# Kernel optimization log

Measured on AMD Instinct MI355X. Metric: run time of the kernel, lower is better.

The kernel has to match this reference:

```python
import jax, jax.numpy as jnp
import numpy as np

N_NODES = 50000
N_EDGES = 1_600_000


def gcn_conv(x, W, b, src, dst, ew, n_nodes):
    """PyG GCNConv: out = D^{-1/2}(A+I)D^{-1/2} (x W) + b, deg from edge_weight,
    self-loop weight = 1. Self-loop term handled analytically (norm = dinv[i]^2)."""
    xW = x @ W                                            # [N, F_out]
    deg = jax.ops.segment_sum(ew, dst, num_segments=n_nodes) + 1.0  # +1 self-loop
    dinv = jnp.where(deg > 0, jax.lax.rsqrt(deg), 0.0)    # [N]
    norm = dinv[src] * ew * dinv[dst]                     # [E]
    agg = jax.ops.segment_sum(norm[:, None] * xW[src], dst, num_segments=n_nodes)
    return agg + (dinv * dinv)[:, None] * xW + b


def setup_inputs() -> dict:
    key = jax.random.key(0)
    ks = jax.random.split(key, 9)
    s = lambda fi, fo: 1.0 / np.sqrt(fi)
    return {
        "x": jax.random.normal(ks[0], (N_NODES, 128), dtype=jnp.float32),
        "edge_index": jax.random.randint(ks[1], (2, N_EDGES), 0, N_NODES, dtype=jnp.int64)
        if jax.config.jax_enable_x64 else jax.random.randint(ks[1], (2, N_EDGES), 0, N_NODES, dtype=jnp.int32),
        "edge_weight": jax.random.uniform(ks[2], (N_EDGES,), dtype=jnp.float32),
        "W1": jax.random.normal(ks[3], (128, 64), dtype=jnp.float32) * s(128, 64),
        "b1": jnp.zeros((64,), dtype=jnp.float32),
        "W2": jax.random.normal(ks[4], (64, 64), dtype=jnp.float32) * s(64, 64),
        "b2": jnp.zeros((64,), dtype=jnp.float32),
        "W3": jax.random.normal(ks[5], (64, 40), dtype=jnp.float32) * s(64, 40),
        "b3": jnp.zeros((40,), dtype=jnp.float32),
    }


def reference(x, edge_index, edge_weight, W1, b1, W2, b2, W3, b3):
    src, dst = edge_index[0], edge_index[1]
    n = x.shape[0]
    h = jax.nn.relu(gcn_conv(x, W1, b1, src, dst, edge_weight, n))
    h = jax.nn.relu(gcn_conv(h, W2, b2, src, dst, edge_weight, n))
    return gcn_conv(h, W3, b3, src, dst, edge_weight, n)
```

## Files before the change

### kernel.cpp

```cpp
#include <hip/hip_runtime.h>


#define TILE 4096
#define BCAP_MAX 9216

static __device__ __forceinline__ float4 f4zero() { return make_float4(0.f, 0.f, 0.f, 0.f); }

static __device__ __forceinline__ unsigned short f2bf_rne(float x) {
    unsigned u = __float_as_uint(x);
    u += 0x7FFFu + ((u >> 16) & 1u);
    return (unsigned short)(u >> 16);
}
static __device__ __forceinline__ float bflo(unsigned u) { return __uint_as_float(u << 16); }
static __device__ __forceinline__ float bfhi(unsigned u) { return __uint_as_float(u & 0xffff0000u); }

__global__ __launch_bounds__(1024) void bin_count_kernel(
        const int* __restrict__ dst, int* __restrict__ cnt, int E, int ntiles) {
    __shared__ int h[256];
    const int tid = threadIdx.x;
    const int t = blockIdx.x;
    if (tid < 256) h[tid] = 0;
    __syncthreads();
    const int e0 = t * TILE;
    #pragma unroll
    for (int j = 0; j < 4; ++j) {
        int e = e0 + j * 1024 + tid;
        if (e < E) atomicAdd(&h[dst[e] >> 8], 1);
    }
    __syncthreads();
    if (tid < 256) cnt[tid * ntiles + t] = h[tid];
}

__global__ __launch_bounds__(512) void bin_scan_kernel(
        int* __restrict__ cnt, int* __restrict__ bintotal, int ntiles) {
    __shared__ int buf[512];
    const int b = blockIdx.x;
    const int tid = threadIdx.x;
    int v = (tid < ntiles) ? cnt[b * ntiles + tid] : 0;
    buf[tid] = v;
    __syncthreads();
    for (int off = 1; off < 512; off <<= 1) {
        int x = buf[tid];
        int a = (tid >= off) ? buf[tid - off] : 0;
        __syncthreads();
        buf[tid] = x + a;
        __syncthreads();
    }
    if (tid < ntiles) cnt[b * ntiles + tid] = buf[tid] - v;
    if (tid == 0) bintotal[b] = buf[511];
}

__global__ __launch_bounds__(1024) void bin_scatter_kernel(
        const int* __restrict__ src, const int* __restrict__ dst,
        const float* __restrict__ ew, const int* __restrict__ cntbase,
        int2* __restrict__ binned, int E, int bcap, int ntiles) {
    __shared__ int cnt[256];
    __shared__ int scan[256];
    __shared__ int gbase[256];
    __shared__ int2 sorted[TILE];
    __shared__ unsigned char binof[TILE];
    const int tid = threadIdx.x;
    const int t = blockIdx.x;
    const int e0 = t * TILE;

    if (tid < 256) cnt[tid] = 0;
    __syncthreads();

    int mypk[4]; float myew[4]; int mybin[4]; int myrank[4]; bool myok[4];
    #pragma unroll
    for (int j = 0; j < 4; ++j) {
        int e = e0 + j * 1024 + tid;
        myok[j] = (e < E);
        if (myok[j]) {
            int d = dst[e];
            int s = src[e];
            myew[j]   = ew[e];
            mybin[j]  = d >> 8;
            mypk[j]   = (s << 8) | (d & 255);
            myrank[j] = atomicAdd(&cnt[mybin[j]], 1);
        }
    }
    __syncthreads();
    if (tid < 256) scan[tid] = cnt[tid];
    __syncthreads();
    for (int off = 1; off < 256; off <<= 1) {
        int v = 0;
        if (tid < 256) { v = scan[tid]; if (tid >= off) v += scan[tid - off]; }
        __syncthreads();
        if (tid < 256) scan[tid] = v;
        __syncthreads();
    }
    if (tid < 256) gbase[tid] = cntbase[tid * ntiles + t];
    __syncthreads();
    #pragma unroll
    for (int j = 0; j < 4; ++j) {
        if (myok[j]) {
            int b = mybin[j];
            int slot = (scan[b] - cnt[b]) + myrank[j];
            sorted[slot] = make_int2(mypk[j], __float_as_int(myew[j]));
            binof[slot]  = (unsigned char)b;
        }
    }
    __syncthreads();
    const int total = scan[255];
    for (int i = tid; i < total; i += 1024) {
        int b = binof[i];
        int pos = gbase[b] + (i - (scan[b] - cnt[b]));
        if (pos < bcap)
            binned[(size_t)b * bcap + pos] = sorted[i];
    }
}

__global__ __launch_bounds__(1024) void bin_group_kernel(
        int2* __restrict__ binned, const int* __restrict__ bintotal,
        int* __restrict__ row_start, int* __restrict__ row_cnt,
        float* __restrict__ dinv, int N, int bcap) {
    __shared__ int   cntl[256];
    __shared__ float degl[256];
    __shared__ int   scan[256];
    __shared__ int   run[256];
    __shared__ int2  sorted[BCAP_MAX];
    const int b = blockIdx.x;
    const int tid = threadIdx.x;
    int n = bintotal[b];
    if (n > bcap) n = bcap;
    if (tid < 256) { cntl[tid] = 0; degl[tid] = 0.f; }
    __syncthreads();

    int2* seg = binned + (size_t)b * bcap;
    for (int i = tid; i < n; i += 1024) {
        int2 v = seg[i];
        int dl = v.x & 255;
        atomicAdd(&cntl[dl], 1);
        atomicAdd(&degl[dl], __int_as_float(v.y));
    }
    __syncthreads();
    if (tid < 256) scan[tid] = cntl[tid];
    __syncthreads();
    for (int off = 1; off < 256; off <<= 1) {
        int v = 0;
        if (tid < 256) { v = scan[tid]; if (tid >= off) v += scan[tid - off]; }
        __syncthreads();
        if (tid < 256) scan[tid] = v;
        __syncthreads();
    }
    if (tid < 256) {
        int ex = scan[tid] - cntl[tid];
        int d = (b << 8) + tid;
        if (d < N) {
            row_start[d] = b * bcap + ex;
            row_cnt[d]   = cntl[tid];
            dinv[d]      = rsqrtf(degl[tid] + 1.0f);
        }
        run[tid] = ex;
    }
    __syncthreads();
    for (int i = tid; i < n; i += 1024) {
        int2 v = seg[i];
        int dl = v.x & 255;
        int r = atomicAdd(&run[dl], 1);
        sorted[r] = make_int2((v.x >> 8) << 7, v.y);
    }
    __syncthreads();
    for (int i = tid; i < n; i += 1024)
        seg[i] = sorted[i];
}

template <int K, int M>
__global__ __launch_bounds__(256) void gemm_kernel(const float* __restrict__ X,
        const float* __restrict__ W, const float* __restrict__ dinv,
        unsigned short* __restrict__ Y, int N) {
    constexpr int KP = K + 4;
    __shared__ float xs[64 * KP];
    __shared__ float ws[K * M];
    const int tid = threadIdx.x;
    const int row0 = blockIdx.x * 64;

    for (int i = tid * 4; i < K * M; i += 1024)
        *(float4*)&ws[i] = *(const float4*)&W[i];

    const int nrows = min(64, N - row0);
    for (int i = tid * 4; i < 64 * K; i += 1024) {
        int r = i / K, k = i % K;
        float4 v = f4zero();
        if (r < nrows) v = *(const float4*)&X[(size_t)(row0 + r) * K + k];
        *(float4*)&xs[r * KP + k] = v;
    }
    __syncthreads();

    const int ct = tid & 15, rt = tid >> 4;
    const int c = ct * 4;
    const bool cok = (c < M);
    float acc[4][4] = {};
    for (int k = 0; k < K; ++k) {
        float a0 = xs[(rt +  0) * KP + k];
        float a1 = xs[(rt + 16) * KP + k];
        float a2 = xs[(rt + 32) * KP + k];
        float a3 = xs[(rt + 48) * KP + k];
        float4 bv = cok ? *(const float4*)&ws[k * M + c] : f4zero();
        acc[0][0] += a0 * bv.x; acc[0][1] += a0 * bv.y; acc[0][2] += a0 * bv.z; acc[0][3] += a0 * bv.w;
        acc[1][0] += a1 * bv.x; acc[1][1] += a1 * bv.y; acc[1][2] += a1 * bv.z; acc[1][3] += a1 * bv.w;
        acc[2][0] += a2 * bv.x; acc[2][1] += a2 * bv.y; acc[2][2] += a2 * bv.z; acc[2][3] += a2 * bv.w;
        acc[3][0] += a3 * bv.x; acc[3][1] += a3 * bv.y; acc[3][2] += a3 * bv.z; acc[3][3] += a3 * bv.w;
    }
    if (cok) {
        #pragma unroll
        for (int i = 0; i < 4; ++i) {
            int r = row0 + rt + 16 * i;
            if (r < N) {
                float dd = dinv[r];
                ushort4 o;
                o.x = f2bf_rne(acc[i][0] * dd); o.y = f2bf_rne(acc[i][1] * dd);
                o.z = f2bf_rne(acc[i][2] * dd); o.w = f2bf_rne(acc[i][3] * dd);
                *(ushort4*)&Y[(size_t)r * 64 + c] = o;
            }
        }
    }
}

template <int FOUT, bool RELU>
__global__ __launch_bounds__(256) void agg_kernel(
        const unsigned short* __restrict__ xw,
        const int2* __restrict__ csr, const int* __restrict__ row_start,
        const int* __restrict__ row_cnt, const float* __restrict__ dinv,
        const float* __restrict__ bias, float* __restrict__ out, int N) {
    int wid = (int)((blockIdx.x * blockDim.x + threadIdx.x) >> 6);
    int lane = threadIdx.x & 63;
    if (wid >= N) return;

    const int2* row = csr + row_start[wid];
    const int   cnt = row_cnt[wid];
    const char* xwb = (const char*)xw;

    const int g = lane >> 3;
    const unsigned li16 = (unsigned)(lane & 7) * 16u;
    const int g4 = g << 2;

    float acc[8] = {0.f, 0.f, 0.f, 0.f, 0.f, 0.f, 0.f, 0.f};

    int2 edA = make_int2(0, 0);
    if (lane < cnt) edA = row[lane];

    for (int base = 0; base < cnt; base += 64) {
        const int m = min(cnt - base, 64);
        int2 edN = make_int2(0, 0);
        const int nb = base + 64;
        if (nb < cnt) {
            if (lane < cnt - nb) edN = row[nb + lane];
        }
        int bidx = g4;
        #pragma unroll 2
        for (int t = 0; t * 8 < m; ++t, bidx += 32) {
            unsigned off = (unsigned)__builtin_amdgcn_ds_bpermute(bidx, edA.x);
            unsigned wu  = (unsigned)__builtin_amdgcn_ds_bpermute(bidx, edA.y);
            const bool valid = (t * 8 + g) < m;
            off = valid ? off : 0u;
            float wf = valid ? __uint_as_float(wu) : 0.f;
            uint4 rv = *(const uint4*)(xwb + (size_t)(off + li16));
            acc[0] = fmaf(wf, bflo(rv.x), acc[0]);
            acc[1] = fmaf(wf, bfhi(rv.x), acc[1]);
            acc[2] = fmaf(wf, bflo(rv.y), acc[2]);
            acc[3] = fmaf(wf, bfhi(rv.y), acc[3]);
            acc[4] = fmaf(wf, bflo(rv.z), acc[4]);
            acc[5] = fmaf(wf, bfhi(rv.z), acc[5]);
            acc[6] = fmaf(wf, bflo(rv.w), acc[6]);
            acc[7] = fmaf(wf, bfhi(rv.w), acc[7]);
        }
        edA = edN;
    }

    #pragma unroll
    for (int o = 8; o <= 32; o <<= 1) {
        #pragma unroll
        for (int t = 0; t < 8; ++t)
            acc[t] += __shfl_xor(acc[t], o);
    }

    if (lane < FOUT / 8) {
        const int f0 = lane * 8;
        uint4 sr = *(const uint4*)(xwb + ((unsigned)wid * 128u + li16));
        float dd = dinv[wid];
        float4 bv0 = *(const float4*)&bias[f0];
        float4 bv1 = *(const float4*)&bias[f0 + 4];
        float r0 = dd * (acc[0] + bflo(sr.x)) + bv0.x;
        float r1 = dd * (acc[1] + bfhi(sr.x)) + bv0.y;
        float r2 = dd * (acc[2] + bflo(sr.y)) + bv0.z;
        float r3 = dd * (acc[3] + bfhi(sr.y)) + bv0.w;
        float r4 = dd * (acc[4] + bflo(sr.z)) + bv1.x;
        float r5 = dd * (acc[5] + bfhi(sr.z)) + bv1.y;
        float r6 = dd * (acc[6] + bflo(sr.w)) + bv1.z;
        float r7 = dd * (acc[7] + bfhi(sr.w)) + bv1.w;
        if (RELU) {
            r0 = fmaxf(r0, 0.f); r1 = fmaxf(r1, 0.f); r2 = fmaxf(r2, 0.f); r3 = fmaxf(r3, 0.f);
            r4 = fmaxf(r4, 0.f); r5 = fmaxf(r5, 0.f); r6 = fmaxf(r6, 0.f); r7 = fmaxf(r7, 0.f);
        }
        *(float4*)&out[(size_t)wid * FOUT + f0]     = make_float4(r0, r1, r2, r3);
        *(float4*)&out[(size_t)wid * FOUT + f0 + 4] = make_float4(r4, r5, r6, r7);
    }
}

static inline size_t ws_align(size_t x) { return (x + 255) & ~(size_t)255; }

extern "C" void kernel_launch(void* const* d_in, const int* in_sizes, int n_in,
                              void* d_out, int out_size, void* d_ws, size_t ws_size,
                              hipStream_t stream) {
    const float* x  = (const float*)d_in[0];
    const int*   ei = (const int*)d_in[1];
    const float* ew = (const float*)d_in[2];
    const float* W1 = (const float*)d_in[3];
    const float* b1 = (const float*)d_in[4];
    const float* W2 = (const float*)d_in[5];
    const float* b2 = (const float*)d_in[6];
    const float* W3 = (const float*)d_in[7];
    const float* b3 = (const float*)d_in[8];
    float* out = (float*)d_out;

    const int N = in_sizes[0] / 128;
    const int E = in_sizes[1] / 2;
    const int* src = ei;
    const int* dst = ei + E;
    const int nbins = (N + 255) >> 8;
    const int ntiles = (E + TILE - 1) / TILE;

    char* p = (char*)d_ws;
    size_t off = 0;
    auto alloc = [&](size_t bytes) -> char* {
        char* q = p + off;
        off = ws_align(off + bytes);
        return q;
    };
    int*   row_start = (int*)  alloc((size_t)N * 4);
    int*   row_cnt   = (int*)  alloc((size_t)N * 4);
    float* dinv      = (float*)alloc((size_t)N * 4);
    int*   cntbase   = (int*)  alloc((size_t)256 * ntiles * 4);
    int*   bintotal  = (int*)  alloc((size_t)256 * 4);
    unsigned short* xwbuf = (unsigned short*)alloc((size_t)N * 64 * 2);
    float* hbuf      = (float*)alloc((size_t)N * 64 * 4);
    size_t remain = (ws_size > off + 512) ? (ws_size - off - 512) : 0;
    int bcap = (int)(remain / ((size_t)nbins * 8));
    if (bcap > BCAP_MAX) bcap = BCAP_MAX;
    int2* binned = (int2*)alloc((size_t)nbins * (size_t)bcap * 8);

    const int gb = (N + 63) / 64;
    const int ab = (N + 3) / 4;

    bin_count_kernel<<<ntiles, 1024, 0, stream>>>(dst, cntbase, E, ntiles);
    bin_scan_kernel<<<256, 512, 0, stream>>>(cntbase, bintotal, ntiles);
    bin_scatter_kernel<<<ntiles, 1024, 0, stream>>>(src, dst, ew, cntbase, binned, E, bcap, ntiles);
    bin_group_kernel<<<nbins, 1024, 0, stream>>>(binned, bintotal, row_start, row_cnt, dinv, N, bcap);

    gemm_kernel<128, 64><<<gb, 256, 0, stream>>>(x, W1, dinv, xwbuf, N);
    agg_kernel<64, true ><<<ab, 256, 0, stream>>>(xwbuf, binned, row_start, row_cnt, dinv, b1, hbuf, N);
    gemm_kernel<64, 64><<<gb, 256, 0, stream>>>(hbuf, W2, dinv, xwbuf, N);
    agg_kernel<64, true ><<<ab, 256, 0, stream>>>(xwbuf, binned, row_start, row_cnt, dinv, b2, hbuf, N);
    gemm_kernel<64, 40><<<gb, 256, 0, stream>>>(hbuf, W3, dinv, xwbuf, N);
    agg_kernel<40, false><<<ab, 256, 0, stream>>>(xwbuf, binned, row_start, row_cnt, dinv, b3, out, N);
}
```

Measured before the change: 269.3 us.

## Replace two-level bin sort with global-atomic CSR build

Replaces the tiled two-level binning (shared-memory histograms, per-bin scan, local scatter and regroup) with a direct CSR construction: global atomic count and degree per node, a single-block exclusive scan, and an atomic-slot scatter. The goal is fewer kernels, fewer passes over the edge list and no capacity-limited bins. In exchange it relies on heavy global atomics to random addresses, a serial one-block scan over all nodes, and edge order within each row that varies from run to run, so float summation order is not deterministic.

```diff
diff --git a/kernel.cpp b/kernel.cpp
--- a/kernel.cpp
+++ b/kernel.cpp
@@ -1,8 +1,5 @@
 #include <hip/hip_runtime.h>
 
-
-#define TILE 4096
-#define BCAP_MAX 9216
 
 static __device__ __forceinline__ float4 f4zero() { return make_float4(0.f, 0.f, 0.f, 0.f); }
 
@@ -14,156 +11,67 @@
 static __device__ __forceinline__ float bflo(unsigned u) { return __uint_as_float(u << 16); }
 static __device__ __forceinline__ float bfhi(unsigned u) { return __uint_as_float(u & 0xffff0000u); }
 
-__global__ __launch_bounds__(1024) void bin_count_kernel(
-        const int* __restrict__ dst, int* __restrict__ cnt, int E, int ntiles) {
-    __shared__ int h[256];
+__global__ __launch_bounds__(1024) void zero_kernel(int* __restrict__ cnt,
+        float* __restrict__ deg, int N) {
+    int i = blockIdx.x * 1024 + threadIdx.x;
+    if (i < N) { cnt[i] = 0; deg[i] = 0.f; }
+}
+
+__global__ __launch_bounds__(1024) void count_kernel(
+        const int* __restrict__ dst, const float* __restrict__ ew,
+        int* __restrict__ cnt, float* __restrict__ deg, int E) {
+    int stride = gridDim.x * 1024;
+    for (int e = blockIdx.x * 1024 + threadIdx.x; e < E; e += stride) {
+        int d = dst[e];
+        atomicAdd(&cnt[d], 1);
+        atomicAdd(&deg[d], ew[e]);
+    }
+}
+
+__global__ __launch_bounds__(1024) void scan_kernel(
+        const int* __restrict__ cnt, const float* __restrict__ deg,
+        int* __restrict__ row_start, int* __restrict__ run,
+        float* __restrict__ dinv, int N) {
+    __shared__ int buf[1024];
     const int tid = threadIdx.x;
-    const int t = blockIdx.x;
-    if (tid < 256) h[tid] = 0;
+    const int P = (N + 1023) >> 10;
+    int s = 0;
+    for (int i = 0; i < P; ++i) {
+        int idx = i * 1024 + tid;
+        if (idx < N) s += cnt[idx];
+    }
+    buf[tid] = s;
     __syncthreads();
-    const int e0 = t * TILE;
-    #pragma unroll
-    for (int j = 0; j < 4; ++j) {
-        int e = e0 + j * 1024 + tid;
-        if (e < E) atomicAdd(&h[dst[e] >> 8], 1);
-    }
-    __syncthreads();
-    if (tid < 256) cnt[tid * ntiles + t] = h[tid];
-}
-
-__global__ __launch_bounds__(512) void bin_scan_kernel(
-        int* __restrict__ cnt, int* __restrict__ bintotal, int ntiles) {
-    __shared__ int buf[512];
-    const int b = blockIdx.x;
-    const int tid = threadIdx.x;
-    int v = (tid < ntiles) ? cnt[b * ntiles + tid] : 0;
-    buf[tid] = v;
-    __syncthreads();
-    for (int off = 1; off < 512; off <<= 1) {
+    for (int off = 1; off < 1024; off <<= 1) {
         int x = buf[tid];
         int a = (tid >= off) ? buf[tid - off] : 0;
         __syncthreads();
         buf[tid] = x + a;
         __syncthreads();
     }
-    if (tid < ntiles) cnt[b * ntiles + tid] = buf[tid] - v;
-    if (tid == 0) bintotal[b] = buf[511];
-}
-
-__global__ __launch_bounds__(1024) void bin_scatter_kernel(
+    int r = buf[tid] - s;
+    for (int i = 0; i < P; ++i) {
+        int idx = i * 1024 + tid;
+        if (idx < N) {
+            int c = cnt[idx];
+            row_start[idx] = r;
+            run[idx]       = r;
+            dinv[idx]      = rsqrtf(deg[idx] + 1.0f);
+            r += c;
+        }
+    }
+}
+
+__global__ __launch_bounds__(1024) void scatter_kernel(
         const int* __restrict__ src, const int* __restrict__ dst,
-        const float* __restrict__ ew, const int* __restrict__ cntbase,
-        int2* __restrict__ binned, int E, int bcap, int ntiles) {
-    __shared__ int cnt[256];
-    __shared__ int scan[256];
-    __shared__ int gbase[256];
-    __shared__ int2 sorted[TILE];
-    __shared__ unsigned char binof[TILE];
-    const int tid = threadIdx.x;
-    const int t = blockIdx.x;
-    const int e0 = t * TILE;
-
-    if (tid < 256) cnt[tid] = 0;
-    __syncthreads();
-
-    int mypk[4]; float myew[4]; int mybin[4]; int myrank[4]; bool myok[4];
-    #pragma unroll
-    for (int j = 0; j < 4; ++j) {
-        int e = e0 + j * 1024 + tid;
-        myok[j] = (e < E);
-        if (myok[j]) {
-            int d = dst[e];
-            int s = src[e];
-            myew[j]   = ew[e];
-            mybin[j]  = d >> 8;
-            mypk[j]   = (s << 8) | (d & 255);
-            myrank[j] = atomicAdd(&cnt[mybin[j]], 1);
-        }
-    }
-    __syncthreads();
-    if (tid < 256) scan[tid] = cnt[tid];
-    __syncthreads();
-    for (int off = 1; off < 256; off <<= 1) {
-        int v = 0;
-        if (tid < 256) { v = scan[tid]; if (tid >= off) v += scan[tid - off]; }
-        __syncthreads();
-        if (tid < 256) scan[tid] = v;
-        __syncthreads();
-    }
-    if (tid < 256) gbase[tid] = cntbase[tid * ntiles + t];
-    __syncthreads();
-    #pragma unroll
-    for (int j = 0; j < 4; ++j) {
-        if (myok[j]) {
-            int b = mybin[j];
-            int slot = (scan[b] - cnt[b]) + myrank[j];
-            sorted[slot] = make_int2(mypk[j], __float_as_int(myew[j]));
-            binof[slot]  = (unsigned char)b;
-        }
-    }
-    __syncthreads();
-    const int total = scan[255];
-    for (int i = tid; i < total; i += 1024) {
-        int b = binof[i];
-        int pos = gbase[b] + (i - (scan[b] - cnt[b]));
-        if (pos < bcap)
-            binned[(size_t)b * bcap + pos] = sorted[i];
-    }
-}
-
-__global__ __launch_bounds__(1024) void bin_group_kernel(
-        int2* __restrict__ binned, const int* __restrict__ bintotal,
-        int* __restrict__ row_start, int* __restrict__ row_cnt,
-        float* __restrict__ dinv, int N, int bcap) {
-    __shared__ int   cntl[256];
-    __shared__ float degl[256];
-    __shared__ int   scan[256];
-    __shared__ int   run[256];
-    __shared__ int2  sorted[BCAP_MAX];
-    const int b = blockIdx.x;
-    const int tid = threadIdx.x;
-    int n = bintotal[b];
-    if (n > bcap) n = bcap;
-    if (tid < 256) { cntl[tid] = 0; degl[tid] = 0.f; }
-    __syncthreads();
-
-    int2* seg = binned + (size_t)b * bcap;
-    for (int i = tid; i < n; i += 1024) {
-        int2 v = seg[i];
-        int dl = v.x & 255;
-        atomicAdd(&cntl[dl], 1);
-        atomicAdd(&degl[dl], __int_as_float(v.y));
-    }
-    __syncthreads();
-    if (tid < 256) scan[tid] = cntl[tid];
-    __syncthreads();
-    for (int off = 1; off < 256; off <<= 1) {
-        int v = 0;
-        if (tid < 256) { v = scan[tid]; if (tid >= off) v += scan[tid - off]; }
-        __syncthreads();
-        if (tid < 256) scan[tid] = v;
-        __syncthreads();
-    }
-    if (tid < 256) {
-        int ex = scan[tid] - cntl[tid];
-        int d = (b << 8) + tid;
-        if (d < N) {
-            row_start[d] = b * bcap + ex;
-            row_cnt[d]   = cntl[tid];
-            dinv[d]      = rsqrtf(degl[tid] + 1.0f);
-        }
-        run[tid] = ex;
-    }
-    __syncthreads();
-    for (int i = tid; i < n; i += 1024) {
-        int2 v = seg[i];
-        int dl = v.x & 255;
-        int r = atomicAdd(&run[dl], 1);
-        sorted[r] = make_int2((v.x >> 8) << 7, v.y);
-    }
-    __syncthreads();
-    for (int i = tid; i < n; i += 1024)
-        seg[i] = sorted[i];
+        const float* __restrict__ ew, int* __restrict__ run,
+        int2* __restrict__ binned, int E) {
+    int stride = gridDim.x * 1024;
+    for (int e = blockIdx.x * 1024 + threadIdx.x; e < E; e += stride) {
+        int d = dst[e];
+        int pos = atomicAdd(&run[d], 1);
+        binned[pos] = make_int2(src[e] << 7, __float_as_int(ew[e]));
+    }
 }
 
 template <int K, int M>
@@ -319,8 +227,6 @@
     const int E = in_sizes[1] / 2;
     const int* src = ei;
     const int* dst = ei + E;
-    const int nbins = (N + 255) >> 8;
-    const int ntiles = (E + TILE - 1) / TILE;
 
     char* p = (char*)d_ws;
     size_t off = 0;
@@ -331,23 +237,22 @@
     };
     int*   row_start = (int*)  alloc((size_t)N * 4);
     int*   row_cnt   = (int*)  alloc((size_t)N * 4);
+    int*   run       = (int*)  alloc((size_t)N * 4);
+    float* deg       = (float*)alloc((size_t)N * 4);
     float* dinv      = (float*)alloc((size_t)N * 4);
-    int*   cntbase   = (int*)  alloc((size_t)256 * ntiles * 4);
-    int*   bintotal  = (int*)  alloc((size_t)256 * 4);
     unsigned short* xwbuf = (unsigned short*)alloc((size_t)N * 64 * 2);
     float* hbuf      = (float*)alloc((size_t)N * 64 * 4);
-    size_t remain = (ws_size > off + 512) ? (ws_size - off - 512) : 0;
-    int bcap = (int)(remain / ((size_t)nbins * 8));
-    if (bcap > BCAP_MAX) bcap = BCAP_MAX;
-    int2* binned = (int2*)alloc((size_t)nbins * (size_t)bcap * 8);
-
+    int2*  binned    = (int2*) alloc((size_t)E * 8);
+
+    const int zb = (N + 1023) / 1024;
+    const int eb = 512;
     const int gb = (N + 63) / 64;
     const int ab = (N + 3) / 4;
 
-    bin_count_kernel<<<ntiles, 1024, 0, stream>>>(dst, cntbase, E, ntiles);
-    bin_scan_kernel<<<256, 512, 0, stream>>>(cntbase, bintotal, ntiles);
-    bin_scatter_kernel<<<ntiles, 1024, 0, stream>>>(src, dst, ew, cntbase, binned, E, bcap, ntiles);
-    bin_group_kernel<<<nbins, 1024, 0, stream>>>(binned, bintotal, row_start, row_cnt, dinv, N, bcap);
+    zero_kernel<<<zb, 1024, 0, stream>>>(row_cnt, deg, N);
+    count_kernel<<<eb, 1024, 0, stream>>>(dst, ew, row_cnt, deg, E);
+    scan_kernel<<<1, 1024, 0, stream>>>(row_cnt, deg, row_start, run, dinv, N);
+    scatter_kernel<<<eb, 1024, 0, stream>>>(src, dst, ew, run, binned, E);
 
     gemm_kernel<128, 64><<<gb, 256, 0, stream>>>(x, W1, dinv, xwbuf, N);
     agg_kernel<64, true ><<<ab, 256, 0, stream>>>(xwbuf, binned, row_start, row_cnt, dinv, b1, hbuf, N);
```

Result: slower. 533.5 us (+98.1%).

## Split bf16 XW into column planes and aggregate each plane in separate passes

Applied to the files above, without the earlier changes.

The GEMM output now goes into two column planes: the first 32 features, then the rest (32 or 8). Each layer's aggregation runs as two passes, one per plane, so each pass gathers a smaller working set (about 3.2 MB for 50k×32 bf16) that fits better in cache for the random neighbour gathers. Edge offsets are stored as row*64 and shifted per plane width. The cost is twice the CSR traversal and kernel launches per layer, and the 8-wide pass gives each lane less work.

```diff
diff --git a/kernel.cpp b/kernel.cpp
--- a/kernel.cpp
+++ b/kernel.cpp
@@ -159,7 +159,7 @@
         int2 v = seg[i];
         int dl = v.x & 255;
         int r = atomicAdd(&run[dl], 1);
-        sorted[r] = make_int2((v.x >> 8) << 7, v.y);
+        sorted[r] = make_int2((v.x >> 8) << 6, v.y);
     }
     __syncthreads();
     for (int i = tid; i < n; i += 1024)
@@ -171,6 +171,7 @@
         const float* __restrict__ W, const float* __restrict__ dinv,
         unsigned short* __restrict__ Y, int N) {
     constexpr int KP = K + 4;
+    constexpr int P1S = (M == 40) ? 8 : 32;
     __shared__ float xs[64 * KP];
     __shared__ float ws[K * M];
     const int tid = threadIdx.x;
@@ -212,29 +213,34 @@
                 ushort4 o;
                 o.x = f2bf_rne(acc[i][0] * dd); o.y = f2bf_rne(acc[i][1] * dd);
                 o.z = f2bf_rne(acc[i][2] * dd); o.w = f2bf_rne(acc[i][3] * dd);
-                *(ushort4*)&Y[(size_t)r * 64 + c] = o;
+                unsigned short* dp;
+                if (c < 32) dp = &Y[(size_t)r * 32 + c];
+                else        dp = &Y[(size_t)N * 32 + (size_t)r * P1S + (c - 32)];
+                *(ushort4*)dp = o;
             }
         }
     }
 }
 
-template <int FOUT, bool RELU>
-__global__ __launch_bounds__(256) void agg_kernel(
-        const unsigned short* __restrict__ xw,
+template <int FH, int FTOT, int COFF, bool RELU>
+__global__ __launch_bounds__(256) void agg_pass_kernel(
+        const unsigned short* __restrict__ plane,
         const int2* __restrict__ csr, const int* __restrict__ row_start,
         const int* __restrict__ row_cnt, const float* __restrict__ dinv,
         const float* __restrict__ bias, float* __restrict__ out, int N) {
+    constexpr int LPR = FH / 8;
+    constexpr int EPS = 64 / LPR;
+    constexpr int SH  = (FH == 32) ? 0 : 2;
     int wid = (int)((blockIdx.x * blockDim.x + threadIdx.x) >> 6);
     int lane = threadIdx.x & 63;
     if (wid >= N) return;
 
     const int2* row = csr + row_start[wid];
     const int   cnt = row_cnt[wid];
-    const char* xwb = (const char*)xw;
-
-    const int g = lane >> 3;
-    const unsigned li16 = (unsigned)(lane & 7) * 16u;
-    const int g4 = g << 2;
+    const char* xwb = (const char*)plane;
+
+    const int g = lane / LPR;
+    const unsigned li16 = (unsigned)(lane % LPR) * 16u;
 
     float acc[8] = {0.f, 0.f, 0.f, 0.f, 0.f, 0.f, 0.f, 0.f};
 
@@ -248,15 +254,22 @@
         if (nb < cnt) {
             if (lane < cnt - nb) edN = row[nb + lane];
         }
-        int bidx = g4;
-        #pragma unroll 2
-        for (int t = 0; t * 8 < m; ++t, bidx += 32) {
-            unsigned off = (unsigned)__builtin_amdgcn_ds_bpermute(bidx, edA.x);
-            unsigned wu  = (unsigned)__builtin_amdgcn_ds_bpermute(bidx, edA.y);
-            const bool valid = (t * 8 + g) < m;
+        #pragma unroll
+        for (int t = 0; t < 64 / EPS; ++t) {
+            if (t * EPS >= m) break;
+            unsigned off, wu;
+            if (EPS == 64) {
+                off = (unsigned)edA.x;
+                wu  = (unsigned)edA.y;
+            } else {
+                int bidx = (t * EPS + g) << 2;
+                off = (unsigned)__builtin_amdgcn_ds_bpermute(bidx, edA.x);
+                wu  = (unsigned)__builtin_amdgcn_ds_bpermute(bidx, edA.y);
+            }
+            const bool valid = (t * EPS + g) < m;
             off = valid ? off : 0u;
             float wf = valid ? __uint_as_float(wu) : 0.f;
-            uint4 rv = *(const uint4*)(xwb + (size_t)(off + li16));
+            uint4 rv = *(const uint4*)(xwb + (size_t)((off >> SH) + li16));
             acc[0] = fmaf(wf, bflo(rv.x), acc[0]);
             acc[1] = fmaf(wf, bfhi(rv.x), acc[1]);
             acc[2] = fmaf(wf, bflo(rv.y), acc[2]);
@@ -270,18 +283,18 @@
     }
 
     #pragma unroll
-    for (int o = 8; o <= 32; o <<= 1) {
+    for (int o = LPR; o <= 32; o <<= 1) {
         #pragma unroll
         for (int t = 0; t < 8; ++t)
             acc[t] += __shfl_xor(acc[t], o);
     }
 
-    if (lane < FOUT / 8) {
+    if (lane < LPR) {
         const int f0 = lane * 8;
-        uint4 sr = *(const uint4*)(xwb + ((unsigned)wid * 128u + li16));
+        uint4 sr = *(const uint4*)(xwb + (size_t)wid * (FH * 2) + (unsigned)lane * 16u);
         float dd = dinv[wid];
-        float4 bv0 = *(const float4*)&bias[f0];
-        float4 bv1 = *(const float4*)&bias[f0 + 4];
+        float4 bv0 = *(const float4*)&bias[COFF + f0];
+        float4 bv1 = *(const float4*)&bias[COFF + f0 + 4];
         float r0 = dd * (acc[0] + bflo(sr.x)) + bv0.x;
         float r1 = dd * (acc[1] + bfhi(sr.x)) + bv0.y;
         float r2 = dd * (acc[2] + bflo(sr.y)) + bv0.z;
@@ -294,8 +307,8 @@
             r0 = fmaxf(r0, 0.f); r1 = fmaxf(r1, 0.f); r2 = fmaxf(r2, 0.f); r3 = fmaxf(r3, 0.f);
             r4 = fmaxf(r4, 0.f); r5 = fmaxf(r5, 0.f); r6 = fmaxf(r6, 0.f); r7 = fmaxf(r7, 0.f);
         }
-        *(float4*)&out[(size_t)wid * FOUT + f0]     = make_float4(r0, r1, r2, r3);
-        *(float4*)&out[(size_t)wid * FOUT + f0 + 4] = make_float4(r4, r5, r6, r7);
+        *(float4*)&out[(size_t)wid * FTOT + COFF + f0]     = make_float4(r0, r1, r2, r3);
+        *(float4*)&out[(size_t)wid * FTOT + COFF + f0 + 4] = make_float4(r4, r5, r6, r7);
     }
 }
 
@@ -336,10 +349,12 @@
     int*   bintotal  = (int*)  alloc((size_t)256 * 4);
     unsigned short* xwbuf = (unsigned short*)alloc((size_t)N * 64 * 2);
     float* hbuf      = (float*)alloc((size_t)N * 64 * 4);
-    size_t remain = (ws_size > off + 512) ? (ws_size - off - 512) : 0;
+    size_t remain = (ws_size > off) ? (ws_size - off) : 0;
     int bcap = (int)(remain / ((size_t)nbins * 8));
     if (bcap > BCAP_MAX) bcap = BCAP_MAX;
     int2* binned = (int2*)alloc((size_t)nbins * (size_t)bcap * 8);
+
+    const unsigned short* plane1 = xwbuf + (size_t)N * 32;
 
     const int gb = (N + 63) / 64;
     const int ab = (N + 3) / 4;
@@ -350,9 +365,12 @@
     bin_group_kernel<<<nbins, 1024, 0, stream>>>(binned, bintotal, row_start, row_cnt, dinv, N, bcap);
 
     gemm_kernel<128, 64><<<gb, 256, 0, stream>>>(x, W1, dinv, xwbuf, N);
-    agg_kernel<64, true ><<<ab, 256, 0, stream>>>(xwbuf, binned, row_start, row_cnt, dinv, b1, hbuf, N);
+    agg_pass_kernel<32, 64,  0, true ><<<ab, 256, 0, stream>>>(xwbuf,  binned, row_start, row_cnt, dinv, b1, hbuf, N);
+    agg_pass_kernel<32, 64, 32, true ><<<ab, 256, 0, stream>>>(plane1, binned, row_start, row_cnt, dinv, b1, hbuf, N);
     gemm_kernel<64, 64><<<gb, 256, 0, stream>>>(hbuf, W2, dinv, xwbuf, N);
-    agg_kernel<64, true ><<<ab, 256, 0, stream>>>(xwbuf, binned, row_start, row_cnt, dinv, b2, hbuf, N);
+    agg_pass_kernel<32, 64,  0, true ><<<ab, 256, 0, stream>>>(xwbuf,  binned, row_start, row_cnt, dinv, b2, hbuf, N);
+    agg_pass_kernel<32, 64, 32, true ><<<ab, 256, 0, stream>>>(plane1, binned, row_start, row_cnt, dinv, b2, hbuf, N);
     gemm_kernel<64, 40><<<gb, 256, 0, stream>>>(hbuf, W3, dinv, xwbuf, N);
-    agg_kernel<40, false><<<ab, 256, 0, stream>>>(xwbuf, binned, row_start, row_cnt, dinv, b3, out, N);
-}
+    agg_pass_kernel<32, 40,  0, false><<<ab, 256, 0, stream>>>(xwbuf,  binned, row_start, row_cnt, dinv, b3, out, N);
+    agg_pass_kernel< 8, 40, 32, false><<<ab, 256, 0, stream>>>(plane1, binned, row_start, row_cnt, dinv, b3, out, N);
+}
```

New measurement: 325.8 us. 1.21x slower.

## Fuse binning kernels into one cooperative kernel with grid syncs

Applied to the files above, without the earlier changes.

Merges the four CSR-building kernels (count, scan, scatter, group) into one cooperative launch. Grid-wide syncs replace the kernel boundaries, and all phases share one statically sized LDS buffer. The aim is to remove the launch and drain gaps between the small preprocessing kernels. In exchange, every phase now reserves the largest LDS footprint, which can lower residency, and grid.sync adds its own overhead. Correctness also depends on all 391 blocks being co-resident.

```diff
diff --git a/kernel.cpp b/kernel.cpp
--- a/kernel.cpp
+++ b/kernel.cpp
@@ -1,4 +1,7 @@
 #include <hip/hip_runtime.h>
+#include <hip/hip_cooperative_groups.h>
+
+namespace cg = cooperative_groups;
 
 
 #define TILE 4096
@@ -14,156 +17,159 @@
 static __device__ __forceinline__ float bflo(unsigned u) { return __uint_as_float(u << 16); }
 static __device__ __forceinline__ float bfhi(unsigned u) { return __uint_as_float(u & 0xffff0000u); }
 
-__global__ __launch_bounds__(1024) void bin_count_kernel(
-        const int* __restrict__ dst, int* __restrict__ cnt, int E, int ntiles) {
-    __shared__ int h[256];
+__global__ __launch_bounds__(1024, 8) void bin_fused_kernel(
+        const int* __restrict__ src, const int* __restrict__ dst,
+        const float* __restrict__ ew, int* __restrict__ cntbase,
+        int* __restrict__ bintotal, int2* __restrict__ binned,
+        int* __restrict__ row_start, int* __restrict__ row_cnt,
+        float* __restrict__ dinv, int E, int N, int bcap, int ntiles, int nbins) {
+    __shared__ __align__(16) char sm[77824];
     const int tid = threadIdx.x;
-    const int t = blockIdx.x;
-    if (tid < 256) h[tid] = 0;
-    __syncthreads();
-    const int e0 = t * TILE;
-    #pragma unroll
-    for (int j = 0; j < 4; ++j) {
-        int e = e0 + j * 1024 + tid;
-        if (e < E) atomicAdd(&h[dst[e] >> 8], 1);
-    }
-    __syncthreads();
-    if (tid < 256) cnt[tid * ntiles + t] = h[tid];
-}
-
-__global__ __launch_bounds__(512) void bin_scan_kernel(
-        int* __restrict__ cnt, int* __restrict__ bintotal, int ntiles) {
-    __shared__ int buf[512];
-    const int b = blockIdx.x;
-    const int tid = threadIdx.x;
-    int v = (tid < ntiles) ? cnt[b * ntiles + tid] : 0;
-    buf[tid] = v;
-    __syncthreads();
-    for (int off = 1; off < 512; off <<= 1) {
-        int x = buf[tid];
-        int a = (tid >= off) ? buf[tid - off] : 0;
-        __syncthreads();
-        buf[tid] = x + a;
-        __syncthreads();
-    }
-    if (tid < ntiles) cnt[b * ntiles + tid] = buf[tid] - v;
-    if (tid == 0) bintotal[b] = buf[511];
-}
-
-__global__ __launch_bounds__(1024) void bin_scatter_kernel(
-        const int* __restrict__ src, const int* __restrict__ dst,
-        const float* __restrict__ ew, const int* __restrict__ cntbase,
-        int2* __restrict__ binned, int E, int bcap, int ntiles) {
-    __shared__ int cnt[256];
-    __shared__ int scan[256];
-    __shared__ int gbase[256];
-    __shared__ int2 sorted[TILE];
-    __shared__ unsigned char binof[TILE];
-    const int tid = threadIdx.x;
-    const int t = blockIdx.x;
-    const int e0 = t * TILE;
-
-    if (tid < 256) cnt[tid] = 0;
-    __syncthreads();
-
-    int mypk[4]; float myew[4]; int mybin[4]; int myrank[4]; bool myok[4];
-    #pragma unroll
-    for (int j = 0; j < 4; ++j) {
-        int e = e0 + j * 1024 + tid;
-        myok[j] = (e < E);
-        if (myok[j]) {
-            int d = dst[e];
-            int s = src[e];
-            myew[j]   = ew[e];
-            mybin[j]  = d >> 8;
-            mypk[j]   = (s << 8) | (d & 255);
-            myrank[j] = atomicAdd(&cnt[mybin[j]], 1);
-        }
-    }
-    __syncthreads();
-    if (tid < 256) scan[tid] = cnt[tid];
-    __syncthreads();
-    for (int off = 1; off < 256; off <<= 1) {
+    const int blk = blockIdx.x;
+    cg::grid_group grid = cg::this_grid();
+
+    {
+        int* h = (int*)sm;
+        if (tid < 256) h[tid] = 0;
+        __syncthreads();
+        const int e0 = blk * TILE;
+        #pragma unroll
+        for (int j = 0; j < 4; ++j) {
+            int e = e0 + j * 1024 + tid;
+            if (e < E) atomicAdd(&h[dst[e] >> 8], 1);
+        }
+        __syncthreads();
+        if (tid < 256) cntbase[tid * ntiles + blk] = h[tid];
+    }
+    grid.sync();
+
+    if (blk < 256) {
+        int* buf = (int*)sm;
         int v = 0;
-        if (tid < 256) { v = scan[tid]; if (tid >= off) v += scan[tid - off]; }
-        __syncthreads();
-        if (tid < 256) scan[tid] = v;
-        __syncthreads();
-    }
-    if (tid < 256) gbase[tid] = cntbase[tid * ntiles + t];
-    __syncthreads();
-    #pragma unroll
-    for (int j = 0; j < 4; ++j) {
-        if (myok[j]) {
-            int b = mybin[j];
-            int slot = (scan[b] - cnt[b]) + myrank[j];
-            sorted[slot] = make_int2(mypk[j], __float_as_int(myew[j]));
-            binof[slot]  = (unsigned char)b;
-        }
-    }
-    __syncthreads();
-    const int total = scan[255];
-    for (int i = tid; i < total; i += 1024) {
-        int b = binof[i];
-        int pos = gbase[b] + (i - (scan[b] - cnt[b]));
-        if (pos < bcap)
-            binned[(size_t)b * bcap + pos] = sorted[i];
-    }
-}
-
-__global__ __launch_bounds__(1024) void bin_group_kernel(
-        int2* __restrict__ binned, const int* __restrict__ bintotal,
-        int* __restrict__ row_start, int* __restrict__ row_cnt,
-        float* __restrict__ dinv, int N, int bcap) {
-    __shared__ int   cntl[256];
-    __shared__ float degl[256];
-    __shared__ int   scan[256];
-    __shared__ int   run[256];
-    __shared__ int2  sorted[BCAP_MAX];
-    const int b = blockIdx.x;
-    const int tid = threadIdx.x;
-    int n = bintotal[b];
-    if (n > bcap) n = bcap;
-    if (tid < 256) { cntl[tid] = 0; degl[tid] = 0.f; }
-    __syncthreads();
-
-    int2* seg = binned + (size_t)b * bcap;
-    for (int i = tid; i < n; i += 1024) {
-        int2 v = seg[i];
-        int dl = v.x & 255;
-        atomicAdd(&cntl[dl], 1);
-        atomicAdd(&degl[dl], __int_as_float(v.y));
-    }
-    __syncthreads();
-    if (tid < 256) scan[tid] = cntl[tid];
-    __syncthreads();
-    for (int off = 1; off < 256; off <<= 1) {
-        int v = 0;
-        if (tid < 256) { v = scan[tid]; if (tid >= off) v += scan[tid - off]; }
-        __syncthreads();
-        if (tid < 256) scan[tid] = v;
-        __syncthreads();
-    }
-    if (tid < 256) {
-        int ex = scan[tid] - cntl[tid];
-        int d = (b << 8) + tid;
-        if (d < N) {
-            row_start[d] = b * bcap + ex;
-            row_cnt[d]   = cntl[tid];
-            dinv[d]      = rsqrtf(degl[tid] + 1.0f);
-        }
-        run[tid] = ex;
-    }
-    __syncthreads();
-    for (int i = tid; i < n; i += 1024) {
-        int2 v = seg[i];
-        int dl = v.x & 255;
-        int r = atomicAdd(&run[dl], 1);
-        sorted[r] = make_int2((v.x >> 8) << 7, v.y);
-    }
-    __syncthreads();
-    for (int i = tid; i < n; i += 1024)
-        seg[i] = sorted[i];
+        if (tid < 512) {
+            v = (tid < ntiles) ? cntbase[blk * ntiles + tid] : 0;
+            buf[tid] = v;
+        }
+        __syncthreads();
+        for (int off = 1; off < 512; off <<= 1) {
+            int x = 0, a = 0;
+            if (tid < 512) { x = buf[tid]; a = (tid >= off) ? buf[tid - off] : 0; }
+            __syncthreads();
+            if (tid < 512) buf[tid] = x + a;
+            __syncthreads();
+        }
+        if (tid < ntiles) cntbase[blk * ntiles + tid] = buf[tid] - v;
+        if (tid == 0) bintotal[blk] = buf[511];
+    }
+    grid.sync();
+
+    {
+        int*  cnt   = (int*)sm;
+        int*  scan  = (int*)(sm + 1024);
+        int*  gbase = (int*)(sm + 2048);
+        int2* sorted = (int2*)(sm + 3072);
+        unsigned char* binof = (unsigned char*)(sm + 3072 + 32768);
+
+        if (tid < 256) cnt[tid] = 0;
+        __syncthreads();
+
+        int mypk[4]; float myew[4]; int mybin[4]; int myrank[4]; bool myok[4];
+        const int e0 = blk * TILE;
+        #pragma unroll
+        for (int j = 0; j < 4; ++j) {
+            int e = e0 + j * 1024 + tid;
+            myok[j] = (e < E);
+            if (myok[j]) {
+                int d = dst[e];
+                int s = src[e];
+                myew[j]   = ew[e];
+                mybin[j]  = d >> 8;
+                mypk[j]   = (s << 8) | (d & 255);
+                myrank[j] = atomicAdd(&cnt[mybin[j]], 1);
+            }
+        }
+        __syncthreads();
+        if (tid < 256) scan[tid] = cnt[tid];
+        __syncthreads();
+        for (int off = 1; off < 256; off <<= 1) {
+            int v = 0;
+            if (tid < 256) { v = scan[tid]; if (tid >= off) v += scan[tid - off]; }
+            __syncthreads();
+            if (tid < 256) scan[tid] = v;
+            __syncthreads();
+        }
+        if (tid < 256) gbase[tid] = cntbase[tid * ntiles + blk];
+        __syncthreads();
+        #pragma unroll
+        for (int j = 0; j < 4; ++j) {
+            if (myok[j]) {
+                int b = mybin[j];
+                int slot = (scan[b] - cnt[b]) + myrank[j];
+                sorted[slot] = make_int2(mypk[j], __float_as_int(myew[j]));
+                binof[slot]  = (unsigned char)b;
+            }
+        }
+        __syncthreads();
+        const int total = scan[255];
+        for (int i = tid; i < total; i += 1024) {
+            int b = binof[i];
+            int pos = gbase[b] + (i - (scan[b] - cnt[b]));
+            if (pos < bcap)
+                binned[(size_t)b * bcap + pos] = sorted[i];
+        }
+    }
+    grid.sync();
+
+    if (blk < nbins) {
+        int*   cntl = (int*)sm;
+        float* degl = (float*)(sm + 1024);
+        int*   scan = (int*)(sm + 2048);
+        int*   run  = (int*)(sm + 3072);
+        int2*  sorted = (int2*)(sm + 4096);
+
+        int n = bintotal[blk];
+        if (n > bcap) n = bcap;
+        if (tid < 256) { cntl[tid] = 0; degl[tid] = 0.f; }
+        __syncthreads();
+
+        int2* seg = binned + (size_t)blk * bcap;
+        for (int i = tid; i < n; i += 1024) {
+            int2 v = seg[i];
+            int dl = v.x & 255;
+            atomicAdd(&cntl[dl], 1);
+            atomicAdd(&degl[dl], __int_as_float(v.y));
+        }
+        __syncthreads();
+        if (tid < 256) scan[tid] = cntl[tid];
+        __syncthreads();
+        for (int off = 1; off < 256; off <<= 1) {
+            int v = 0;
+            if (tid < 256) { v = scan[tid]; if (tid >= off) v += scan[tid - off]; }
+            __syncthreads();
+            if (tid < 256) scan[tid] = v;
+            __syncthreads();
+        }
+        if (tid < 256) {
+            int ex = scan[tid] - cntl[tid];
+            int d = (blk << 8) + tid;
+            if (d < N) {
+                row_start[d] = blk * bcap + ex;
+                row_cnt[d]   = cntl[tid];
+                dinv[d]      = rsqrtf(degl[tid] + 1.0f);
+            }
+            run[tid] = ex;
+        }
+        __syncthreads();
+        for (int i = tid; i < n; i += 1024) {
+            int2 v = seg[i];
+            int dl = v.x & 255;
+            int r = atomicAdd(&run[dl], 1);
+            sorted[r] = make_int2((v.x >> 8) << 7, v.y);
+        }
+        __syncthreads();
+        for (int i = tid; i < n; i += 1024)
+            seg[i] = sorted[i];
+    }
 }
 
 template <int K, int M>
@@ -336,7 +342,7 @@
     int*   bintotal  = (int*)  alloc((size_t)256 * 4);
     unsigned short* xwbuf = (unsigned short*)alloc((size_t)N * 64 * 2);
     float* hbuf      = (float*)alloc((size_t)N * 64 * 4);
-    size_t remain = (ws_size > off + 512) ? (ws_size - off - 512) : 0;
+    size_t remain = (ws_size > off) ? (ws_size - off) : 0;
     int bcap = (int)(remain / ((size_t)nbins * 8));
     if (bcap > BCAP_MAX) bcap = BCAP_MAX;
     int2* binned = (int2*)alloc((size_t)nbins * (size_t)bcap * 8);
@@ -344,10 +350,17 @@
     const int gb = (N + 63) / 64;
     const int ab = (N + 3) / 4;
 
-    bin_count_kernel<<<ntiles, 1024, 0, stream>>>(dst, cntbase, E, ntiles);
-    bin_scan_kernel<<<256, 512, 0, stream>>>(cntbase, bintotal, ntiles);
-    bin_scatter_kernel<<<ntiles, 1024, 0, stream>>>(src, dst, ew, cntbase, binned, E, bcap, ntiles);
-    bin_group_kernel<<<nbins, 1024, 0, stream>>>(binned, bintotal, row_start, row_cnt, dinv, N, bcap);
+    {
+        int E_ = E, N_ = N, bcap_ = bcap, ntiles_ = ntiles, nbins_ = nbins;
+        const int* src_ = src; const int* dst_ = dst; const float* ew_ = ew;
+        int* cntbase_ = cntbase; int* bintotal_ = bintotal; int2* binned_ = binned;
+        int* row_start_ = row_start; int* row_cnt_ = row_cnt; float* dinv_ = dinv;
+        void* args[] = { &src_, &dst_, &ew_, &cntbase_, &bintotal_, &binned_,
+                         &row_start_, &row_cnt_, &dinv_, &E_, &N_, &bcap_,
+                         &ntiles_, &nbins_ };
+        hipLaunchCooperativeKernel((const void*)bin_fused_kernel,
+                                   dim3(ntiles), dim3(1024), args, 0, stream);
+    }
 
     gemm_kernel<128, 64><<<gb, 256, 0, stream>>>(x, W1, dinv, xwbuf, N);
     agg_kernel<64, true ><<<ab, 256, 0, stream>>>(xwbuf, binned, row_start, row_cnt, dinv, b1, hbuf, N);
```

After: 418.0 us. 1.55x slower.
